# Kernel optimization log

Measured on AMD Instinct MI355X. Metric: run time of the kernel, lower is better.

Reference implementation:

```python
import jax, jax.numpy as jnp
import numpy as np


def setup_inputs() -> dict:
    key = jax.random.key(0)
    k1, k2 = jax.random.split(key)
    B, D, T = 8, 256, 4096
    Q, K = 8, 1024
    z = jax.random.normal(k1, (B, D, T), dtype=jnp.float32)
    # original init: uniform(-1/n_e, 1/n_e)
    codebooks = jax.random.uniform(k2, (Q, K, D), dtype=jnp.float32,
                                   minval=-1.0 / K, maxval=1.0 / K)
    return {"z": z, "codebooks": codebooks}


def reference(z, codebooks):
    # z: [B, e_dim, T]; codebooks: [Q, n_e, e_dim]
    zp = jnp.transpose(z, (0, 2, 1))  # [B, T, D]
    residual = zp
    quantized_out = jnp.zeros_like(zp)
    total_loss = jnp.zeros((), dtype=z.dtype)
    all_indices = []
    Q = codebooks.shape[0]
    for q in range(Q):  # small fixed number of residual stages
        E = codebooks[q]  # [K, D]
        # squared euclidean distances: ||r||^2 + ||e||^2 - 2 r.e
        d = (jnp.sum(residual ** 2, axis=-1, keepdims=True)
             + jnp.sum(E ** 2, axis=-1)
             - 2.0 * jnp.einsum('btd,kd->btk', residual, E))  # [B, T, K]
        idx = jnp.argmin(d, axis=-1)  # [B, T]
        z_q = E[idx]                  # [B, T, D] gather
        loss = (jnp.mean((jax.lax.stop_gradient(z_q) - residual) ** 2)
                + 0.25 * jnp.mean((z_q - jax.lax.stop_gradient(residual)) ** 2))
        # straight-through estimator
        z_q_st = residual + jax.lax.stop_gradient(z_q - residual)
        residual = residual - z_q_st
        quantized_out = quantized_out + z_q_st
        total_loss = total_loss + loss
        all_indices.append(idx)
    quantized_out = jnp.transpose(quantized_out, (0, 2, 1))  # [B, D, T]
    return quantized_out, total_loss, jnp.stack(all_indices)  # indices: [Q, B, T]
```

## Files before the change

### kernel.cpp

```cpp
#include <hip/hip_runtime.h>

#define B_   8
#define D_   256
#define T_   4096
#define Q_   8
#define K_   1024
#define BT_  (B_*T_)
#define N_   (B_*T_*D_)
#define LOSS_OFF N_
#define IDX_OFF  (N_+1)
#define ROWS 32

typedef __attribute__((ext_vector_type(8))) short short8;
typedef __attribute__((ext_vector_type(4))) float float4v;

union U4S8 { uint4 u; short8 s; };

__device__ __forceinline__ unsigned short f2bf(float x) {
    unsigned int u = __float_as_uint(x);
    unsigned int r = (u + 0x7FFFu + ((u >> 16) & 1u)) >> 16;
    return (unsigned short)r;
}
__device__ __forceinline__ float bf2f(unsigned short b) {
    return __uint_as_float(((unsigned int)b) << 16);
}
__device__ __forceinline__ unsigned fkey(float f) {
    unsigned u = __float_as_uint(f);
    return (u & 0x80000000u) ? ~u : (u | 0x80000000u);
}
__device__ __forceinline__ float fkeyinv(unsigned k) {
    unsigned u = (k & 0x80000000u) ? (k & 0x7fffffffu) : ~k;
    return __uint_as_float(u);
}


__global__ void k_init(const float* __restrict__ z, float* __restrict__ residual,
                       double* lossAcc) {
    __shared__ float tile[32][33];
    int b  = blockIdx.z;
    int d0 = blockIdx.y * 32;
    int t0 = blockIdx.x * 32;
    int tx = threadIdx.x & 31;
    int ty = threadIdx.x >> 5;
    const float* zb = z + (size_t)b * D_ * T_;
    #pragma unroll
    for (int r = 0; r < 32; r += 8)
        tile[ty + r][tx] = zb[(size_t)(d0 + ty + r) * T_ + t0 + tx];
    __syncthreads();
    float* rb = residual + (size_t)b * T_ * D_;
    #pragma unroll
    for (int r = 0; r < 32; r += 8)
        rb[(size_t)(t0 + ty + r) * D_ + d0 + tx] = tile[tx][ty + r];
    if (b == 0 && blockIdx.x == 0 && blockIdx.y == 0 && threadIdx.x == 0)
        *lossAcc = 0.0;
}


__global__ void k_bfrag(const float* __restrict__ cb, uint4* __restrict__ Bfrag) {
    int gid = blockIdx.x * 256 + threadIdx.x;
    int q    = gid >> 15;
    int rem  = gid & 32767;
    int ct   = rem >> 9;
    int kc   = (rem >> 6) & 7;
    int lane = rem & 63;
    int cand = ct * 16 + (lane & 15);
    int kb   = kc * 32 + (lane >> 4) * 8;
    const float* e = cb + ((size_t)q * K_ + cand) * D_ + kb;
    float4v u0 = *(const float4v*)(e);
    float4v u1 = *(const float4v*)(e + 4);
    float vv[8] = {u0.x, u0.y, u0.z, u0.w, u1.x, u1.y, u1.z, u1.w};
    unsigned short h[8], l[8];
    #pragma unroll
    for (int j = 0; j < 8; ++j) {
        float v = vv[j];
        h[j] = f2bf(v);
        l[j] = f2bf(v - bf2f(h[j]));
    }
    uint4 hi, lo;
    hi.x = (unsigned)h[0] | ((unsigned)h[1] << 16);
    hi.y = (unsigned)h[2] | ((unsigned)h[3] << 16);
    hi.z = (unsigned)h[4] | ((unsigned)h[5] << 16);
    hi.w = (unsigned)h[6] | ((unsigned)h[7] << 16);
    lo.x = (unsigned)l[0] | ((unsigned)l[1] << 16);
    lo.y = (unsigned)l[2] | ((unsigned)l[3] << 16);
    lo.z = (unsigned)l[4] | ((unsigned)l[5] << 16);
    lo.w = (unsigned)l[6] | ((unsigned)l[7] << 16);
    size_t base = (((size_t)(q * 64 + ct) * 8 + kc) * 2) * 64;
    Bfrag[base + lane]      = hi;
    Bfrag[base + 64 + lane] = lo;
}


__global__ void k_se(const float* __restrict__ cb, float* __restrict__ Se) {
    int gid = blockIdx.x * 256 + threadIdx.x;
    int i  = gid >> 4;
    int ln = gid & 15;
    if (i >= Q_ * K_) return;
    const float* e = cb + (size_t)i * D_ + ln * 16;
    float4v v0 = *(const float4v*)(e);
    float4v v1 = *(const float4v*)(e + 4);
    float4v v2 = *(const float4v*)(e + 8);
    float4v v3 = *(const float4v*)(e + 12);
    float vv[16] = {v0.x, v0.y, v0.z, v0.w, v1.x, v1.y, v1.z, v1.w,
                    v2.x, v2.y, v2.z, v2.w, v3.x, v3.y, v3.z, v3.w};
    double s = 0.0;
    #pragma unroll
    for (int d = 0; d < 16; ++d) {
        float a = vv[d] * vv[d];
        s += (double)a;
    }
    #pragma unroll
    for (int st = 8; st > 0; st >>= 1) s += __shfl_xor(s, st);
    if (ln == 0) Se[i] = (float)s;
}


__launch_bounds__(512, 2)
__global__ void k_stage(const float* __restrict__ cb,
                        const uint4* __restrict__ Bfrag,
                        const float* __restrict__ Se,
                        float* __restrict__ residual,
                        float* __restrict__ out,
                        double* __restrict__ lossAcc,
                        int q) {
    __shared__ union {
        uint4 afr[2048];
        struct { int slist[32][16]; float sdd[32][16];
                 int srow[512]; int sslot[512]; } post;
        struct { float ovd[512]; int ovk[512]; } over;
        double lred[8];
    } sc;
    __shared__ float seL[1024];
    __shared__ float srb[32], margin[32];
    __shared__ unsigned sminI[32];
    __shared__ int   scount[32], sidx[32];
    __shared__ int   nSurv;

    const int tid  = threadIdx.x;
    const int lane = tid & 63;
    const int w    = tid >> 6;
    const int quad = lane >> 4;
    const int lc   = lane & 15;
    const int row0 = blockIdx.x * ROWS;
    const int g    = tid >> 8;
    const int dt   = tid & 255;

    if (tid < 32) { scount[tid] = 0; sminI[tid] = 0xFFFFFFFFu; }
    if (tid == 32) nSurv = 0;
    seL[tid]       = Se[q * K_ + tid];
    seL[tid + 512] = Se[q * K_ + tid + 512];

    const uint4* __restrict__ Bq = Bfrag + (size_t)q * (64 * 8 * 2 * 64);
    U4S8 b0h, b0l, b1h, b1l;
    {
        const uint4* p0 = Bq + (((size_t)((w * 8 + 0) * 8 + 0)) * 2) * 64 + lane;
        b0h.u = p0[0]; b0l.u = p0[64];
        const uint4* p1 = Bq + (((size_t)((w * 8 + 1) * 8 + 0)) * 2) * 64 + lane;
        b1h.u = p1[0]; b1l.u = p1[64];
    }

    {
        int row = tid >> 4, seg = tid & 15;
        int rg = row >> 4, rlo = row & 15;
        int kc = seg >> 1, par = seg & 1;
        const float* rp = residual + (size_t)(row0 + row) * D_ + seg * 16;
        float4v v0 = *(const float4v*)(rp);
        float4v v1 = *(const float4v*)(rp + 4);
        float4v v2 = *(const float4v*)(rp + 8);
        float4v v3 = *(const float4v*)(rp + 12);
        float vv[16] = {v0.x, v0.y, v0.z, v0.w, v1.x, v1.y, v1.z, v1.w,
                        v2.x, v2.y, v2.z, v2.w, v3.x, v3.y, v3.z, v3.w};
        double s = 0.0; float sa = 0.0f;
        #pragma unroll
        for (int i = 0; i < 16; ++i) {
            float v = vv[i];
            s += (double)(v * v);
            sa += fabsf(v);
        }
        #pragma unroll
        for (int st = 8; st > 0; st >>= 1) {
            s  += __shfl_xor(s, st);
            sa += __shfl_xor(sa, st);
        }
        if (seg == 0) {
            float sr = (float)s;
            float sb = sa * 1.001f;
            srb[row]    = sr;
            margin[row] = 9.6e-7f * sr + 4.0e-7f * sb + 2.0e-4f;
        }
        #pragma unroll
        for (int h = 0; h < 2; ++h) {
            unsigned short hh[8], ll[8];
            #pragma unroll
            for (int j = 0; j < 8; ++j) {
                float v = vv[h * 8 + j];
                hh[j] = f2bf(v);
                ll[j] = f2bf(v - bf2f(hh[j]));
            }
            uint4 hiW, loW;
            hiW.x = (unsigned)hh[0] | ((unsigned)hh[1] << 16);
            hiW.y = (unsigned)hh[2] | ((unsigned)hh[3] << 16);
            hiW.z = (unsigned)hh[4] | ((unsigned)hh[5] << 16);
            hiW.w = (unsigned)hh[6] | ((unsigned)hh[7] << 16);
            loW.x = (unsigned)ll[0] | ((unsigned)ll[1] << 16);
            loW.y = (unsigned)ll[2] | ((unsigned)ll[3] << 16);
            loW.z = (unsigned)ll[4] | ((unsigned)ll[5] << 16);
            loW.w = (unsigned)ll[6] | ((unsigned)ll[7] << 16);
            int ln = (par * 2 + h) * 16 + rlo;
            int sl = ln ^ kc;
            sc.afr[((rg * 8 + kc) * 2 + 0) * 64 + sl] = hiW;
            sc.afr[((rg * 8 + kc) * 2 + 1) * 64 + sl] = loW;
        }
    }
    __syncthreads();

    float4v accA[16];
    #pragma unroll
    for (int i = 0; i < 16; ++i) accA[i] = (float4v){0.f, 0.f, 0.f, 0.f};

    for (int kc = 0; kc < 8; ++kc) {
        U4S8 a0h, a0l, a1h, a1l;
        a0h.u = sc.afr[((0 * 8 + kc) * 2 + 0) * 64 + (lane ^ kc)];
        a0l.u = sc.afr[((0 * 8 + kc) * 2 + 1) * 64 + (lane ^ kc)];
        a1h.u = sc.afr[((1 * 8 + kc) * 2 + 0) * 64 + (lane ^ kc)];
        a1l.u = sc.afr[((1 * 8 + kc) * 2 + 1) * 64 + (lane ^ kc)];
        #pragma unroll
        for (int ctl = 0; ctl < 8; ++ctl) {
            U4S8 bh, bl;
            if ((ctl & 1) == 0) { bh = b0h; bl = b0l; }
            else                { bh = b1h; bl = b1l; }
            {
                int pkc  = kc + ((ctl + 2) >> 3);
                int pctl = (ctl + 2) & 7;
                const uint4* p = Bq + (((size_t)((w * 8 + pctl) * 8 + pkc)) * 2) * 64 + lane;
                if ((ctl & 1) == 0) { b0h.u = p[0]; b0l.u = p[64]; }
                else                { b1h.u = p[0]; b1l.u = p[64]; }
            }
            float4v a0 = accA[ctl * 2 + 0];
            a0 = __builtin_amdgcn_mfma_f32_16x16x32_bf16(a0h.s, bh.s, a0, 0, 0, 0);
            a0 = __builtin_amdgcn_mfma_f32_16x16x32_bf16(a0l.s, bh.s, a0, 0, 0, 0);
            a0 = __builtin_amdgcn_mfma_f32_16x16x32_bf16(a0h.s, bl.s, a0, 0, 0, 0);
            accA[ctl * 2 + 0] = a0;
            float4v a1 = accA[ctl * 2 + 1];
            a1 = __builtin_amdgcn_mfma_f32_16x16x32_bf16(a1h.s, bh.s, a1, 0, 0, 0);
            a1 = __builtin_amdgcn_mfma_f32_16x16x32_bf16(a1l.s, bh.s, a1, 0, 0, 0);
            a1 = __builtin_amdgcn_mfma_f32_16x16x32_bf16(a1h.s, bl.s, a1, 0, 0, 0);
            accA[ctl * 2 + 1] = a1;
        }
    }

    float sr8[8];
    #pragma unroll
    for (int rr = 0; rr < 8; ++rr)
        sr8[rr] = srb[(rr >> 2) * 16 + quad * 4 + (rr & 3)];

    float mn[8];
    #pragma unroll
    for (int rr = 0; rr < 8; ++rr) mn[rr] = 3.4e38f;
    #pragma unroll
    for (int ctl = 0; ctl < 8; ++ctl) {
        int cand = (w * 8 + ctl) * 16 + lc;
        float se = seL[cand];
        #pragma unroll
        for (int rr = 0; rr < 8; ++rr) {
            float dd = (sr8[rr] + se) - 2.0f * accA[ctl * 2 + (rr >> 2)][rr & 3];
            mn[rr] = fminf(mn[rr], dd);
        }
    }
    #pragma unroll
    for (int rr = 0; rr < 8; ++rr) {
        float v = mn[rr];
        v = fminf(v, __shfl_xor(v, 1));
        v = fminf(v, __shfl_xor(v, 2));
        v = fminf(v, __shfl_xor(v, 4));
        v = fminf(v, __shfl_xor(v, 8));
        if (lc == 0)
            atomicMin(&sminI[(rr >> 2) * 16 + quad * 4 + (rr & 3)], fkey(v));
    }
    __syncthreads();

    float thrV[8];
    #pragma unroll
    for (int rr = 0; rr < 8; ++rr) {
        int row = (rr >> 2) * 16 + quad * 4 + (rr & 3);
        thrV[rr] = fkeyinv(sminI[row]) + margin[row];
    }
    #pragma unroll
    for (int ctl = 0; ctl < 8; ++ctl) {
        int cand = (w * 8 + ctl) * 16 + lc;
        float se = seL[cand];
        #pragma unroll
        for (int rr = 0; rr < 8; ++rr) {
            int row = (rr >> 2) * 16 + quad * 4 + (rr & 3);
            float dd = (sr8[rr] + se) - 2.0f * accA[ctl * 2 + (rr >> 2)][rr & 3];
            if (dd <= thrV[rr]) {
                int p = atomicAdd(&scount[row], 1);
                if (p < 16) sc.post.slist[row][p] = cand;
            }
        }
    }
    __syncthreads();

    if (tid < 32) {
        int cnt = scount[tid];
        if (cnt == 1) {
            sidx[tid] = sc.post.slist[tid][0];
        } else if (cnt >= 2 && cnt <= 16) {
            int base = atomicAdd(&nSurv, cnt);
            for (int s2 = 0; s2 < cnt; ++s2) {
                sc.post.srow[base + s2]  = tid;
                sc.post.sslot[base + s2] = s2;
            }
        }
    }
    __syncthreads();

    {
        int nS  = nSurv;
        int grp = tid >> 4, ln = tid & 15;
        for (int j = grp; j < nS; j += 32) {
            int row  = sc.post.srow[j];
            int slot = sc.post.sslot[j];
            int k    = sc.post.slist[row][slot];
            const float* Ek = cb + ((size_t)q * K_ + k) * D_ + ln * 16;
            const float* Rk = residual + (size_t)(row0 + row) * D_ + ln * 16;
            float4v e0 = *(const float4v*)(Ek);
            float4v e1 = *(const float4v*)(Ek + 4);
            float4v e2 = *(const float4v*)(Ek + 8);
            float4v e3 = *(const float4v*)(Ek + 12);
            float4v r0 = *(const float4v*)(Rk);
            float4v r1 = *(const float4v*)(Rk + 4);
            float4v r2 = *(const float4v*)(Rk + 8);
            float4v r3 = *(const float4v*)(Rk + 12);
            float ev[16] = {e0.x, e0.y, e0.z, e0.w, e1.x, e1.y, e1.z, e1.w,
                            e2.x, e2.y, e2.z, e2.w, e3.x, e3.y, e3.z, e3.w};
            float rv2[16] = {r0.x, r0.y, r0.z, r0.w, r1.x, r1.y, r1.z, r1.w,
                             r2.x, r2.y, r2.z, r2.w, r3.x, r3.y, r3.z, r3.w};
            double a0 = 0.0, a1 = 0.0;
            #pragma unroll
            for (int d = 0; d < 16; d += 2) {
                a0 = fma((double)ev[d],     (double)rv2[d],     a0);
                a1 = fma((double)ev[d + 1], (double)rv2[d + 1], a1);
            }
            double ssum = a0 + a1;
            #pragma unroll
            for (int st = 8; st > 0; st >>= 1) ssum += __shfl_xor(ssum, st);
            if (ln == 0) {
                float dotf = (float)ssum;
                float V = srb[row] + seL[k];
                sc.post.sdd[row][slot] = V - 2.0f * dotf;
            }
        }
    }
    __syncthreads();
    if (tid < 32) {
        int cnt = scount[tid];
        if (cnt >= 2 && cnt <= 16) {
            float bd = 3.4e38f; int bk = 0x7fffffff;
            for (int s2 = 0; s2 < cnt; ++s2) {
                float dv = sc.post.sdd[tid][s2]; int kv = sc.post.slist[tid][s2];
                if (dv < bd || (dv == bd && kv < bk)) { bd = dv; bk = kv; }
            }
            sidx[tid] = bk;
        }
    }
    __syncthreads();

    for (int row = 0; row < ROWS; ++row) {
        int cnt = scount[row];
        if (cnt <= 16) continue;
        const float* Rr = residual + (size_t)(row0 + row) * D_;
        float bd = 3.4e38f; int bk = K_;
        #pragma unroll
        for (int c = 0; c < 2; ++c) {
            int k = tid * 2 + c;
            const float* Ek = cb + ((size_t)q * K_ + k) * D_;
            double a0 = 0.0, a1 = 0.0;
            for (int d = 0; d < D_; d += 2) {
                a0 = fma((double)Ek[d],     (double)Rr[d],     a0);
                a1 = fma((double)Ek[d + 1], (double)Rr[d + 1], a1);
            }
            float dd = (srb[row] + seL[k]) - 2.0f * (float)(a0 + a1);
            if (dd < bd || (dd == bd && k < bk)) { bd = dd; bk = k; }
        }
        sc.over.ovd[tid] = bd; sc.over.ovk[tid] = bk;
        __syncthreads();
        for (int st = 256; st > 0; st >>= 1) {
            if (tid < st) {
                float od = sc.over.ovd[tid + st]; int ok = sc.over.ovk[tid + st];
                if (od < sc.over.ovd[tid] ||
                    (od == sc.over.ovd[tid] && ok < sc.over.ovk[tid])) {
                    sc.over.ovd[tid] = od; sc.over.ovk[tid] = ok;
                }
            }
            __syncthreads();
        }
        if (tid == 0) sidx[row] = sc.over.ovk[0];
        __syncthreads();
    }

    const float* Eq = cb + (size_t)q * K_ * D_;
    double lsum = 0.0;
    #pragma unroll
    for (int jj = 0; jj < 16; ++jj) {
        int row = g * 16 + jj;
        int idx = sidx[row];
        size_t roff = (size_t)(row0 + row) * D_ + dt;
        float rv   = residual[roff];
        float zq   = Eq[(size_t)idx * D_ + dt];
        float t1   = zq - rv;
        float zqst = rv + t1;
        residual[roff] = rv - zqst;
        lsum += (double)t1 * (double)t1;
    }
    if (tid < 32) out[IDX_OFF + q * BT_ + row0 + tid] = (float)sidx[tid];

    #pragma unroll
    for (int st = 32; st > 0; st >>= 1) lsum += __shfl_xor(lsum, st);
    __syncthreads();
    if (lane == 0) sc.lred[w] = lsum;
    __syncthreads();
    if (tid == 0) {
        double t = 0.0;
        #pragma unroll
        for (int i = 0; i < 8; ++i) t += sc.lred[i];
        atomicAdd(lossAcc, t);
    }
}


__global__ void k_emit(const float* __restrict__ z, const float* __restrict__ residual,
                       float* __restrict__ out) {
    __shared__ float tile[32][33];
    int b  = blockIdx.z;
    int t0 = blockIdx.y * 32;
    int d0 = blockIdx.x * 32;
    int tx = threadIdx.x & 31;
    int ty = threadIdx.x >> 5;
    const float* rb = residual + (size_t)b * T_ * D_;
    #pragma unroll
    for (int r = 0; r < 32; r += 8)
        tile[ty + r][tx] = rb[(size_t)(t0 + ty + r) * D_ + d0 + tx];
    __syncthreads();
    const float* zb = z + (size_t)b * D_ * T_;
    float* ob = out + (size_t)b * D_ * T_;
    #pragma unroll
    for (int r = 0; r < 32; r += 8) {
        size_t off = (size_t)(d0 + ty + r) * T_ + t0 + tx;
        ob[off] = zb[off] - tile[tx][ty + r];
    }
}

__global__ void k_final(const double* lossAcc, float* out) {
    if (threadIdx.x == 0 && blockIdx.x == 0) {
        double m = *lossAcc / (double)N_;
        out[LOSS_OFF] = (float)(1.25 * m);
    }
}


extern "C" void kernel_launch(void* const* d_in, const int* in_sizes, int n_in,
                              void* d_out, int out_size, void* d_ws, size_t ws_size,
                              hipStream_t stream) {
    const float* z  = (const float*)d_in[0];
    const float* cb = (const float*)d_in[1];
    float* out = (float*)d_out;

    float*  residual = (float*)d_ws;
    uint4*  Bfrag    = (uint4*)((char*)d_ws + (size_t)N_ * 4);
    float*  Se       = (float*)((char*)d_ws + (size_t)N_ * 4 + (size_t)8 * 1024 * 1024);
    double* lossAcc  = (double*)((char*)d_ws + (size_t)N_ * 4 + (size_t)8 * 1024 * 1024
                                 + (size_t)Q_ * K_ * 4);

    hipLaunchKernelGGL(k_init, dim3(T_ / 32, D_ / 32, B_), dim3(256), 0, stream,
                       z, residual, lossAcc);
    hipLaunchKernelGGL(k_bfrag, dim3(1024), dim3(256), 0, stream, cb, Bfrag);
    hipLaunchKernelGGL(k_se, dim3((Q_ * K_ * 16 + 255) / 256), dim3(256), 0, stream,
                       cb, Se);
    for (int q = 0; q < Q_; ++q) {
        hipLaunchKernelGGL(k_stage, dim3(BT_ / ROWS), dim3(512), 0, stream,
                           cb, Bfrag, Se, residual, out, lossAcc, q);
    }
    hipLaunchKernelGGL(k_emit, dim3(D_ / 32, T_ / 32, B_), dim3(256), 0, stream,
                       z, residual, out);
    hipLaunchKernelGGL(k_final, dim3(1), dim3(256), 0, stream, lossAcc, out);
}
```

Before: 818.0 us.

## Drop codebook low-part MFMA term and widen candidate margin by its error bound

The distance GEMM now uses the residual hi/lo split against only the bf16-high part of the codebook, removing one of three MFMAs per tile and the loads of the codebook low fragments. To keep argmin exact, each codebook's maximum squared bf16 rounding error is computed in k_se via atomicMax. The per-row refinement margin grows by a Cauchy-Schwarz bound proportional to sqrt(max error) times the residual norm. This cuts MFMA work and B-fragment traffic, but more candidates may enter the exact fp32 rescoring path.

```diff
diff --git a/kernel.cpp b/kernel.cpp
--- a/kernel.cpp
+++ b/kernel.cpp
@@ -35,7 +35,7 @@
 
 
 __global__ void k_init(const float* __restrict__ z, float* __restrict__ residual,
-                       double* lossAcc) {
+                       double* lossAcc, unsigned* MelU) {
     __shared__ float tile[32][33];
     int b  = blockIdx.z;
     int d0 = blockIdx.y * 32;
@@ -51,8 +51,11 @@
     #pragma unroll
     for (int r = 0; r < 32; r += 8)
         rb[(size_t)(t0 + ty + r) * D_ + d0 + tx] = tile[tx][ty + r];
-    if (b == 0 && blockIdx.x == 0 && blockIdx.y == 0 && threadIdx.x == 0)
+    if (b == 0 && blockIdx.x == 0 && blockIdx.y == 0 && threadIdx.x == 0) {
         *lossAcc = 0.0;
+        #pragma unroll
+        for (int i = 0; i < Q_; ++i) MelU[i] = 0u;
+    }
 }
 
 
@@ -91,7 +94,8 @@
 }
 
 
-__global__ void k_se(const float* __restrict__ cb, float* __restrict__ Se) {
+__global__ void k_se(const float* __restrict__ cb, float* __restrict__ Se,
+                     unsigned* __restrict__ MelU) {
     int gid = blockIdx.x * 256 + threadIdx.x;
     int i  = gid >> 4;
     int ln = gid & 15;
@@ -103,15 +107,24 @@
     float4v v3 = *(const float4v*)(e + 12);
     float vv[16] = {v0.x, v0.y, v0.z, v0.w, v1.x, v1.y, v1.z, v1.w,
                     v2.x, v2.y, v2.z, v2.w, v3.x, v3.y, v3.z, v3.w};
-    double s = 0.0;
+    double s = 0.0, s2 = 0.0;
     #pragma unroll
     for (int d = 0; d < 16; ++d) {
-        float a = vv[d] * vv[d];
+        float v = vv[d];
+        float a = v * v;
         s += (double)a;
-    }
-    #pragma unroll
-    for (int st = 8; st > 0; st >>= 1) s += __shfl_xor(s, st);
-    if (ln == 0) Se[i] = (float)s;
+        float el = v - bf2f(f2bf(v));
+        s2 += (double)(el * el);
+    }
+    #pragma unroll
+    for (int st = 8; st > 0; st >>= 1) {
+        s  += __shfl_xor(s, st);
+        s2 += __shfl_xor(s2, st);
+    }
+    if (ln == 0) {
+        Se[i] = (float)s;
+        atomicMax(&MelU[i >> 10], __float_as_uint((float)s2));
+    }
 }
 
 
@@ -119,6 +132,7 @@
 __global__ void k_stage(const float* __restrict__ cb,
                         const uint4* __restrict__ Bfrag,
                         const float* __restrict__ Se,
+                        const float* __restrict__ Mel,
                         float* __restrict__ residual,
                         float* __restrict__ out,
                         double* __restrict__ lossAcc,
@@ -149,14 +163,15 @@
     if (tid == 32) nSurv = 0;
     seL[tid]       = Se[q * K_ + tid];
     seL[tid + 512] = Se[q * K_ + tid + 512];
+    const float melq4 = 4.04f * sqrtf(Mel[q]);
 
     const uint4* __restrict__ Bq = Bfrag + (size_t)q * (64 * 8 * 2 * 64);
-    U4S8 b0h, b0l, b1h, b1l;
+    U4S8 b0h, b1h;
     {
         const uint4* p0 = Bq + (((size_t)((w * 8 + 0) * 8 + 0)) * 2) * 64 + lane;
-        b0h.u = p0[0]; b0l.u = p0[64];
+        b0h.u = p0[0];
         const uint4* p1 = Bq + (((size_t)((w * 8 + 1) * 8 + 0)) * 2) * 64 + lane;
-        b1h.u = p1[0]; b1l.u = p1[64];
+        b1h.u = p1[0];
     }
 
     {
@@ -186,7 +201,8 @@
             float sr = (float)s;
             float sb = sa * 1.001f;
             srb[row]    = sr;
-            margin[row] = 9.6e-7f * sr + 4.0e-7f * sb + 2.0e-4f;
+            margin[row] = 9.6e-7f * sr + 4.0e-7f * sb + 2.0e-4f
+                        + melq4 * sqrtf(sr);
         }
         #pragma unroll
         for (int h = 0; h < 2; ++h) {
@@ -226,25 +242,21 @@
         a1l.u = sc.afr[((1 * 8 + kc) * 2 + 1) * 64 + (lane ^ kc)];
         #pragma unroll
         for (int ctl = 0; ctl < 8; ++ctl) {
-            U4S8 bh, bl;
-            if ((ctl & 1) == 0) { bh = b0h; bl = b0l; }
-            else                { bh = b1h; bl = b1l; }
+            U4S8 bh = ((ctl & 1) == 0) ? b0h : b1h;
             {
                 int pkc  = kc + ((ctl + 2) >> 3);
                 int pctl = (ctl + 2) & 7;
                 const uint4* p = Bq + (((size_t)((w * 8 + pctl) * 8 + pkc)) * 2) * 64 + lane;
-                if ((ctl & 1) == 0) { b0h.u = p[0]; b0l.u = p[64]; }
-                else                { b1h.u = p[0]; b1l.u = p[64]; }
+                if ((ctl & 1) == 0) b0h.u = p[0];
+                else                b1h.u = p[0];
             }
             float4v a0 = accA[ctl * 2 + 0];
             a0 = __builtin_amdgcn_mfma_f32_16x16x32_bf16(a0h.s, bh.s, a0, 0, 0, 0);
             a0 = __builtin_amdgcn_mfma_f32_16x16x32_bf16(a0l.s, bh.s, a0, 0, 0, 0);
-            a0 = __builtin_amdgcn_mfma_f32_16x16x32_bf16(a0h.s, bl.s, a0, 0, 0, 0);
             accA[ctl * 2 + 0] = a0;
             float4v a1 = accA[ctl * 2 + 1];
             a1 = __builtin_amdgcn_mfma_f32_16x16x32_bf16(a1h.s, bh.s, a1, 0, 0, 0);
             a1 = __builtin_amdgcn_mfma_f32_16x16x32_bf16(a1l.s, bh.s, a1, 0, 0, 0);
-            a1 = __builtin_amdgcn_mfma_f32_16x16x32_bf16(a1h.s, bl.s, a1, 0, 0, 0);
             accA[ctl * 2 + 1] = a1;
         }
     }
@@ -471,15 +483,16 @@
     float*  Se       = (float*)((char*)d_ws + (size_t)N_ * 4 + (size_t)8 * 1024 * 1024);
     double* lossAcc  = (double*)((char*)d_ws + (size_t)N_ * 4 + (size_t)8 * 1024 * 1024
                                  + (size_t)Q_ * K_ * 4);
+    unsigned* MelU   = (unsigned*)((char*)lossAcc + 8);
 
     hipLaunchKernelGGL(k_init, dim3(T_ / 32, D_ / 32, B_), dim3(256), 0, stream,
-                       z, residual, lossAcc);
+                       z, residual, lossAcc, MelU);
     hipLaunchKernelGGL(k_bfrag, dim3(1024), dim3(256), 0, stream, cb, Bfrag);
     hipLaunchKernelGGL(k_se, dim3((Q_ * K_ * 16 + 255) / 256), dim3(256), 0, stream,
-                       cb, Se);
+                       cb, Se, MelU);
     for (int q = 0; q < Q_; ++q) {
         hipLaunchKernelGGL(k_stage, dim3(BT_ / ROWS), dim3(512), 0, stream,
-                           cb, Bfrag, Se, residual, out, lossAcc, q);
+                           cb, Bfrag, Se, (const float*)MelU, residual, out, lossAcc, q);
     }
     hipLaunchKernelGGL(k_emit, dim3(D_ / 32, T_ / 32, B_), dim3(256), 0, stream,
                        z, residual, out);
```

Result: slower. 915.6 us (+11.9%).
